# Kernel optimization log

Measured on AMD Instinct MI355X. Metric: run time of the kernel, lower is better.

Reference implementation:

```python
import jax, jax.numpy as jnp
import numpy as np

H = 1024      # hidden_size
NH = 16       # num_heads
HD = H // NH  # head_dim
MLP_DIM = 4096
EPS = 1e-6


def setup_inputs() -> dict:
    key = jax.random.key(0)
    ks = jax.random.split(key, 16)
    B, S = 8, 1024
    s_in = 1.0 / np.sqrt(H)
    s_mlp = 1.0 / np.sqrt(MLP_DIM)
    return {
        "x": jax.random.normal(ks[0], (B, S, H), jnp.float32),
        "ln1_g": jnp.ones((H,), jnp.float32),
        "ln1_b": jnp.zeros((H,), jnp.float32),
        "Wq": jax.random.normal(ks[1], (H, H), jnp.float32) * s_in,
        "bq": jnp.zeros((H,), jnp.float32),
        "Wk": jax.random.normal(ks[2], (H, H), jnp.float32) * s_in,
        "bk": jnp.zeros((H,), jnp.float32),
        "Wv": jax.random.normal(ks[3], (H, H), jnp.float32) * s_in,
        "bv": jnp.zeros((H,), jnp.float32),
        "Wo": jax.random.normal(ks[4], (H, H), jnp.float32) * s_in,
        "bo": jnp.zeros((H,), jnp.float32),
        "ln2_g": jnp.ones((H,), jnp.float32),
        "ln2_b": jnp.zeros((H,), jnp.float32),
        "W1": jax.random.normal(ks[5], (H, MLP_DIM), jnp.float32) * s_in,
        "b1": jnp.zeros((MLP_DIM,), jnp.float32),
        "W2": jax.random.normal(ks[6], (MLP_DIM, H), jnp.float32) * s_mlp,
        "b2": jnp.zeros((H,), jnp.float32),
    }


def _layernorm(x, g, b):
    mu = jnp.mean(x, axis=-1, keepdims=True)
    var = jnp.mean(jnp.square(x - mu), axis=-1, keepdims=True)
    return (x - mu) * jax.lax.rsqrt(var + EPS) * g + b


def reference(x, ln1_g, ln1_b, Wq, bq, Wk, bk, Wv, bv, Wo, bo,
              ln2_g, ln2_b, W1, b1, W2, b2):
    B, S, _ = x.shape
    # pre-LN attention
    h = _layernorm(x, ln1_g, ln1_b)
    q = (h @ Wq + bq).reshape(B, S, NH, HD).transpose(0, 2, 1, 3)  # bhsd
    k = (h @ Wk + bk).reshape(B, S, NH, HD).transpose(0, 2, 1, 3)
    v = (h @ Wv + bv).reshape(B, S, NH, HD).transpose(0, 2, 1, 3)
    scale = HD ** -0.5
    scores = jnp.einsum('bhqd,bhkd->bhqk', q, k) * scale
    weights = jax.nn.softmax(scores, axis=-1)
    attended = jnp.einsum('bhqk,bhkd->bhqd', weights, v)
    attended = attended.transpose(0, 2, 1, 3).reshape(B, S, H)
    x = x + attended @ Wo + bo
    # pre-LN MLP
    h = _layernorm(x, ln2_g, ln2_b)
    h = jax.nn.gelu(h @ W1 + b1, approximate=False)
    x = x + h @ W2 + b2
    return x
```

## Files before the change

### kernel.cpp

```cpp
#include <hip/hip_runtime.h>

#define H_DIM 1024
#define NHEADS 16
#define HD 64
#define SEQ 1024
#define BATCH 8
#define ROWS (BATCH*SEQ)
#define MLPD 4096

typedef __bf16 bf16x8 __attribute__((ext_vector_type(8)));
typedef float f32x4 __attribute__((ext_vector_type(4)));

__device__ __forceinline__ unsigned short f2bf(float f) {
    unsigned u = __float_as_uint(f);
    unsigned r = u + 0x7FFFu + ((u >> 16) & 1u);
    return (unsigned short)(r >> 16);
}

__global__ void transpose_all(const float* __restrict__ Wq, const float* __restrict__ Wk,
                              const float* __restrict__ Wv, const float* __restrict__ Wo,
                              const float* __restrict__ W1, const float* __restrict__ W2,
                              unsigned short* __restrict__ WqT, unsigned short* __restrict__ WkT,
                              unsigned short* __restrict__ WvT, unsigned short* __restrict__ WoT,
                              unsigned short* __restrict__ W1T, unsigned short* __restrict__ W2T)
{
    __shared__ float tile[32][33];
    const int id = blockIdx.x;
    const float* in; unsigned short* outp; int K, N, t;
    if (id < 4096) {
        const int wsel = id >> 10; t = id & 1023;
        in   = (wsel == 0) ? Wq  : (wsel == 1) ? Wk  : (wsel == 2) ? Wv  : Wo;
        outp = (wsel == 0) ? WqT : (wsel == 1) ? WkT : (wsel == 2) ? WvT : WoT;
        K = 1024; N = 1024;
    } else if (id < 8192) {
        t = id - 4096; in = W1; outp = W1T; K = 1024; N = 4096;
    } else {
        t = id - 8192; in = W2; outp = W2T; K = 4096; N = 1024;
    }
    const int ntx = N >> 5;
    const int n0 = (t % ntx) * 32, k0 = (t / ntx) * 32;
    const int tx = threadIdx.x, ty = threadIdx.y;
    #pragma unroll
    for (int i = ty; i < 32; i += 8)
        tile[i][tx] = in[(size_t)(k0 + i) * N + n0 + tx];
    __syncthreads();
    #pragma unroll
    for (int i = ty; i < 32; i += 8)
        outp[(size_t)(n0 + i) * K + k0 + tx] = f2bf(tile[tx][i]);
}

__global__ void transpose_v(const unsigned short* __restrict__ in,
                            unsigned short* __restrict__ out)
{
    __shared__ unsigned short tile[32][33];
    const size_t base = (size_t)blockIdx.z * (SEQ * HD);
    const int d0 = blockIdx.x * 32, s0 = blockIdx.y * 32;
    const int tx = threadIdx.x, ty = threadIdx.y;
    #pragma unroll
    for (int i = ty; i < 32; i += 8)
        tile[i][tx] = in[base + (size_t)(s0 + i) * HD + d0 + tx];
    __syncthreads();
    const int fx = ((tx & 12) << 1) | ((tx & 16) >> 2) | (tx & 3);
    #pragma unroll
    for (int i = ty; i < 32; i += 8)
        out[base + (size_t)(d0 + i) * SEQ + s0 + fx] = tile[tx][i];
}

__global__ __launch_bounds__(256) void ln_kernel(const float* __restrict__ x,
    const float* __restrict__ g, const float* __restrict__ b,
    unsigned short* __restrict__ out)
{
    __shared__ float red[4];
    const int row = blockIdx.x;
    const int tid = threadIdx.x;
    const float4 v = *(const float4*)(x + (size_t)row * H_DIM + tid * 4);
    float s = v.x + v.y + v.z + v.w;
    #pragma unroll
    for (int off = 32; off >= 1; off >>= 1) s += __shfl_xor(s, off);
    if ((tid & 63) == 0) red[tid >> 6] = s;
    __syncthreads();
    const float mu = (red[0] + red[1] + red[2] + red[3]) * (1.0f / H_DIM);
    __syncthreads();
    const float dx = v.x - mu, dy = v.y - mu, dz = v.z - mu, dw = v.w - mu;
    float q = dx * dx + dy * dy + dz * dz + dw * dw;
    #pragma unroll
    for (int off = 32; off >= 1; off >>= 1) q += __shfl_xor(q, off);
    if ((tid & 63) == 0) red[tid >> 6] = q;
    __syncthreads();
    const float var = (red[0] + red[1] + red[2] + red[3]) * (1.0f / H_DIM);
    const float rstd = rsqrtf(var + 1e-6f);
    const float4 gv = *(const float4*)(g + tid * 4);
    const float4 bv = *(const float4*)(b + tid * 4);
    ushort4 o;
    o.x = f2bf(dx * rstd * gv.x + bv.x);
    o.y = f2bf(dy * rstd * gv.y + bv.y);
    o.z = f2bf(dz * rstd * gv.z + bv.z);
    o.w = f2bf(dw * rstd * gv.w + bv.w);
    *(ushort4*)(out + (size_t)row * H_DIM + tid * 4) = o;
}

template<int MODE>
__global__ __launch_bounds__(256) void gemm_dp(
    const unsigned short* __restrict__ A, const unsigned short* __restrict__ Bt,
    const float* __restrict__ bias0, const float* __restrict__ bias1,
    const float* __restrict__ bias2, const float* resid,
    float* outF, unsigned short* __restrict__ outH,
    int N, int K, int gn)
{
    __shared__ __align__(16) unsigned short As[128 * 128];
    __shared__ __align__(16) unsigned short Bs[128 * 128];

    const int tid = threadIdx.x, lane = tid & 63;
    const int w = tid >> 6;
    const int wm = w >> 1, wn = w & 1;

    const int nwg = gridDim.x;
    const int swzb = (blockIdx.x & 7) * (nwg >> 3) + (blockIdx.x >> 3);
    const int bm = swzb / gn, bn = swzb % gn;

    const int srow = tid >> 4;
    const int sc = (tid & 15) ^ (srow & 7);
    const unsigned short* Abase = A  + (size_t)(bm * 128) * K;
    const unsigned short* Bbase = Bt + (size_t)(bn * 128) * K;

    auto stage = [&](int kt) {
        const size_t kofs = (size_t)kt * 128 + sc * 8;
        #pragma unroll
        for (int q = 0; q < 8; ++q)
            __builtin_amdgcn_global_load_lds(
                (__attribute__((address_space(1))) void*)(Abase + (size_t)(q * 16 + srow) * K + kofs),
                (__attribute__((address_space(3))) void*)(&As[q * 2048 + tid * 8]), 16, 0, 0);
        #pragma unroll
        for (int q = 0; q < 8; ++q)
            __builtin_amdgcn_global_load_lds(
                (__attribute__((address_space(1))) void*)(Bbase + (size_t)(q * 16 + srow) * K + kofs),
                (__attribute__((address_space(3))) void*)(&Bs[q * 2048 + tid * 8]), 16, 0, 0);
    };

    const int lr = lane & 15, hk = lane >> 4, sx = lr & 7;
    const int arow = (wm * 64 + lr) * 128;
    const int brow = (wn * 64 + lr) * 128;

    f32x4 acc[4][4] = {};
    const int nkt = K >> 7;

    for (int t = 0; t < nkt; ++t) {
        stage(t);
        __syncthreads();

        const unsigned short* Ab = &As[arow];
        const unsigned short* Bb = &Bs[brow];

        #pragma unroll
        for (int ks = 0; ks < 4; ++ks) {
            const int px = ((ks * 4 + hk) ^ sx) * 8;
            bf16x8 a[4], b[4];
            #pragma unroll
            for (int i = 0; i < 4; ++i) { b[i] = *(const bf16x8*)(Bb + i * 2048 + px);
                                          a[i] = *(const bf16x8*)(Ab + i * 2048 + px); }
            __builtin_amdgcn_s_setprio(1);
            #pragma unroll
            for (int mi = 0; mi < 4; ++mi)
                #pragma unroll
                for (int ni = 0; ni < 4; ++ni)
                    acc[mi][ni] = __builtin_amdgcn_mfma_f32_16x16x32_bf16(a[mi], b[ni], acc[mi][ni], 0, 0, 0);
            __builtin_amdgcn_s_setprio(0);
        }
        __syncthreads();
    }

    #pragma unroll
    for (int mi = 0; mi < 4; ++mi) {
        #pragma unroll
        for (int ni = 0; ni < 4; ++ni) {
            const int gcol = bn * 128 + wn * 64 + ni * 16 + lr;
            #pragma unroll
            for (int r = 0; r < 4; ++r) {
                const int grow = bm * 128 + wm * 64 + mi * 16 + hk * 4 + r;
                if (MODE == 0) {
                    const int which = gcol >> 10;
                    const int col = gcol & 1023;
                    const float* bp = (which == 0) ? bias0 : (which == 1) ? bias1 : bias2;
                    const float v = acc[mi][ni][r] + bp[col];
                    const int b_ = grow >> 10, s_ = grow & 1023, h_ = col >> 6, d_ = col & 63;
                    outH[(size_t)which * (ROWS * 1024) +
                         (size_t)(b_ * NHEADS + h_) * 65536 + s_ * 64 + d_] = f2bf(v);
                } else if (MODE == 2) {
                    const float v = acc[mi][ni][r] + bias0[gcol];
                    const size_t idx = (size_t)grow * N + gcol;
                    outF[idx] = resid[idx] + v;
                }
            }
        }
    }
}

template<int MODE, int BN>
__global__ __launch_bounds__(512) void gemm_kp(
    const unsigned short* __restrict__ A, const unsigned short* __restrict__ Bt,
    const float* __restrict__ bias0, const float* __restrict__ bias1,
    const float* __restrict__ bias2, const float* resid,
    float* outF, unsigned short* __restrict__ outH,
    int N, int K, int gn)
{
    constexpr int WN = (BN == 256) ? 4 : 2;
    constexpr int WM = 8 / WN;
    constexpr int RM = 256 / WM;
    constexpr int RN = BN / WN;
    constexpr int MR = RM / 16;
    constexpr int NR = RN / 16;
    constexpr int BJ = BN / 128;

    __shared__ __align__(16) unsigned short As[2][2][8192];
    __shared__ __align__(16) unsigned short Bs[2][2][BN * 32];

    const int tid = threadIdx.x, lane = tid & 63;
    const int w = tid >> 6;
    const int wm = w / WN, wn = w % WN;

    const int nwg = gridDim.x;
    const int swzb = (blockIdx.x & 7) * (nwg >> 3) + (blockIdx.x >> 3);
    const int bm = swzb / gn, bn = swzb % gn;

    const unsigned short* Abase = A  + (size_t)(bm * 256) * K;
    const unsigned short* Bbase = Bt + (size_t)(bn * BN) * K;

    int asrow[2], asoff[2];
    #pragma unroll
    for (int j = 0; j < 2; ++j) {
        const int slot = j * 512 + tid;
        asrow[j] = slot >> 2;
        asoff[j] = ((slot & 3) ^ ((asrow[j] >> 1) & 3)) * 8;
    }
    int bsrow[BJ], bsoff[BJ];
    #pragma unroll
    for (int j = 0; j < BJ; ++j) {
        const int slot = j * 512 + tid;
        bsrow[j] = slot >> 2;
        bsoff[j] = ((slot & 3) ^ ((bsrow[j] >> 1) & 3)) * 8;
    }

    auto stageKH = [&](int buf, int kt, int s) {
        #pragma unroll
        for (int j = 0; j < 2; ++j)
            __builtin_amdgcn_global_load_lds(
                (__attribute__((address_space(1))) void*)(Abase + (size_t)asrow[j] * K + (size_t)kt * 64 + s * 32 + asoff[j]),
                (__attribute__((address_space(3))) void*)(&As[buf][s][(j * 512 + tid) * 8]), 16, 0, 0);
        #pragma unroll
        for (int j = 0; j < BJ; ++j)
            __builtin_amdgcn_global_load_lds(
                (__attribute__((address_space(1))) void*)(Bbase + (size_t)bsrow[j] * K + (size_t)kt * 64 + s * 32 + bsoff[j]),
                (__attribute__((address_space(3))) void*)(&Bs[buf][s][(j * 512 + tid) * 8]), 16, 0, 0);
    };

    const int lr = lane & 15, hk = lane >> 4;
    int aoff[MR], boff[NR];
    #pragma unroll
    for (int mf = 0; mf < MR; ++mf) {
        const int R = wm * RM + mf * 16 + lr;
        aoff[mf] = R * 32 + ((hk ^ ((R >> 1) & 3)) * 8);
    }
    #pragma unroll
    for (int nf = 0; nf < NR; ++nf) {
        const int R = wn * RN + nf * 16 + lr;
        boff[nf] = R * 32 + ((hk ^ ((R >> 1) & 3)) * 8);
    }

    f32x4 acc[MR][NR] = {};
    const int nkt = K >> 6;

    stageKH(0, 0, 0);
    stageKH(0, 0, 1);
    if constexpr (BJ == 2) asm volatile("s_waitcnt vmcnt(4)" ::: "memory");
    else                   asm volatile("s_waitcnt vmcnt(3)" ::: "memory");
    __builtin_amdgcn_s_barrier();
    asm volatile("" ::: "memory");

    for (int t = 0; t < nkt; ++t) {
        const int buf = t & 1;
        #pragma unroll
        for (int s = 0; s < 2; ++s) {
            const unsigned short* Ar = &As[buf][s][0];
            const unsigned short* Br = &Bs[buf][s][0];
            bf16x8 af[MR], bf[NR];
            #pragma unroll
            for (int nf = 0; nf < NR; ++nf) bf[nf] = *(const bf16x8*)(Br + boff[nf]);
            #pragma unroll
            for (int mf = 0; mf < MR; ++mf) af[mf] = *(const bf16x8*)(Ar + aoff[mf]);

            if (t + 1 < nkt) {
                stageKH(buf ^ 1, t + 1, s);
                if constexpr (BJ == 2) asm volatile("s_waitcnt vmcnt(4)" ::: "memory");
                else                   asm volatile("s_waitcnt vmcnt(3)" ::: "memory");
            } else {
                asm volatile("s_waitcnt vmcnt(0)" ::: "memory");
            }
            __builtin_amdgcn_s_barrier();
            asm volatile("" ::: "memory");

            __builtin_amdgcn_s_setprio(1);
            #pragma unroll
            for (int mf = 0; mf < MR; ++mf)
                #pragma unroll
                for (int nf = 0; nf < NR; ++nf)
                    acc[mf][nf] = __builtin_amdgcn_mfma_f32_16x16x32_bf16(af[mf], bf[nf], acc[mf][nf], 0, 0, 0);
            __builtin_amdgcn_s_setprio(0);
        }
    }

    #pragma unroll
    for (int mf = 0; mf < MR; ++mf) {
        #pragma unroll
        for (int nf = 0; nf < NR; ++nf) {
            const int gcol = bn * BN + wn * RN + nf * 16 + lr;
            #pragma unroll
            for (int r = 0; r < 4; ++r) {
                const int grow = bm * 256 + wm * RM + mf * 16 + hk * 4 + r;
                if (MODE == 0) {
                    const int which = gcol >> 10;
                    const int col = gcol & 1023;
                    const float* bp = (which == 0) ? bias0 : (which == 1) ? bias1 : bias2;
                    const float v = acc[mf][nf][r] + bp[col];
                    const int b_ = grow >> 10, s_ = grow & 1023, h_ = col >> 6, d_ = col & 63;
                    outH[(size_t)which * (ROWS * 1024) +
                         (size_t)(b_ * NHEADS + h_) * 65536 + s_ * 64 + d_] = f2bf(v);
                } else if (MODE == 2) {
                    const float v = acc[mf][nf][r] + bias0[gcol];
                    const size_t idx = (size_t)grow * N + gcol;
                    outF[idx] = resid[idx] + v;
                } else {
                    const float v = acc[mf][nf][r] + bias0[gcol];
                    const float t3 = fmaf(0.044715f * v * v, v, v);
                    const float e  = __builtin_amdgcn_exp2f(-2.3022086f * t3);
                    const float ge = v * __builtin_amdgcn_rcpf(1.0f + e);
                    outH[(size_t)grow * N + gcol] = f2bf(ge);
                }
            }
        }
    }
}

__global__ __launch_bounds__(256) void attn_kernel(const unsigned short* __restrict__ q,
    const unsigned short* __restrict__ k, const unsigned short* __restrict__ vT,
    unsigned short* __restrict__ out)
{
    __shared__ __align__(16) unsigned short Ks[2][4096];
    __shared__ __align__(16) unsigned short Vs[2][4096];
    const int tid = threadIdx.x, lane = tid & 63, w = tid >> 6;
    const int bh = blockIdx.y;
    const int q0 = blockIdx.x * 256;
    const size_t headBase = (size_t)bh * (SEQ * HD);

    const int qr = lane & 15;
    bf16x8 qf[4][2];
    #pragma unroll
    for (int g = 0; g < 4; ++g) {
        const unsigned short* qp = q + headBase
            + (size_t)(q0 + w * 64 + g * 16 + qr) * HD + (lane >> 4) * 8;
        qf[g][0] = *(const bf16x8*)(qp);
        qf[g][1] = *(const bf16x8*)(qp + 32);
    }

    float lacc[4] = {0.f, 0.f, 0.f, 0.f};
    f32x4 oacc[4][4] = {};

    const int srow = tid >> 3;
    const int swz  = ((tid & 7) ^ (srow & 7)) * 8;
    const int pc   = (lane >> 4) ^ (lane & 7);

    auto stage = [&](int buf, int kt) {
        #pragma unroll
        for (int s = 0; s < 2; ++s) {
            const unsigned short* gk = k  + headBase + (size_t)(kt + s * 32 + srow) * HD + swz;
            const unsigned short* gv = vT + headBase + (size_t)(s * 32 + srow) * SEQ + kt + swz;
            __builtin_amdgcn_global_load_lds((__attribute__((address_space(1))) void*)gk,
                (__attribute__((address_space(3))) void*)(&Ks[buf][s * 2048 + w * 512]), 16, 0, 0);
            __builtin_amdgcn_global_load_lds((__attribute__((address_space(1))) void*)gv,
                (__attribute__((address_space(3))) void*)(&Vs[buf][s * 2048 + w * 512]), 16, 0, 0);
        }
    };

    stage(0, 0);
    __syncthreads();

    const float C1 = 0.125f * 1.44269504f;
    const float C2 = -4.0f * 1.44269504f;

    for (int t = 0; t < 16; ++t) {
        const int cur = t & 1;
        if (t < 15) stage(cur ^ 1, (t + 1) * 64);

        const unsigned short* KB = &Ks[cur][0];
        const unsigned short* VB = &Vs[cur][0];

        #pragma unroll
        for (int g = 0; g < 4; ++g) {
            f32x4 s4[4] = {};
            __builtin_amdgcn_s_setprio(1);
            #pragma unroll
            for (int ni = 0; ni < 4; ++ni) {
                const unsigned short* pk = KB + (ni * 16 + qr) * 64;
                s4[ni] = __builtin_amdgcn_mfma_f32_16x16x32_bf16(*(const bf16x8*)(pk + pc * 8),       qf[g][0], s4[ni], 0, 0, 0);
                s4[ni] = __builtin_amdgcn_mfma_f32_16x16x32_bf16(*(const bf16x8*)(pk + (pc ^ 4) * 8), qf[g][1], s4[ni], 0, 0, 0);
            }
            __builtin_amdgcn_s_setprio(0);

            unsigned U[4][2];
            float ls = 0.f;
            #pragma unroll
            for (int ni = 0; ni < 4; ++ni) {
                const float p0 = __builtin_amdgcn_exp2f(fmaf(s4[ni][0], C1, C2));
                const float p1 = __builtin_amdgcn_exp2f(fmaf(s4[ni][1], C1, C2));
                const float p2 = __builtin_amdgcn_exp2f(fmaf(s4[ni][2], C1, C2));
                const float p3 = __builtin_amdgcn_exp2f(fmaf(s4[ni][3], C1, C2));
                ls += (p0 + p1) + (p2 + p3);
                asm("v_cvt_pk_bf16_f32 %0, %1, %2" : "=v"(U[ni][0]) : "v"(p0), "v"(p1));
                asm("v_cvt_pk_bf16_f32 %0, %1, %2" : "=v"(U[ni][1]) : "v"(p2), "v"(p3));
            }
            lacc[g] += ls;

            union { unsigned u[4]; bf16x8 v; } W0, W1;
            W0.u[0] = U[0][0]; W0.u[1] = U[0][1]; W0.u[2] = U[1][0]; W0.u[3] = U[1][1];
            W1.u[0] = U[2][0]; W1.u[1] = U[2][1]; W1.u[2] = U[3][0]; W1.u[3] = U[3][1];

            __builtin_amdgcn_s_setprio(1);
            #pragma unroll
            for (int nd = 0; nd < 4; ++nd) {
                const unsigned short* pv = VB + (nd * 16 + qr) * 64;
                oacc[g][nd] = __builtin_amdgcn_mfma_f32_16x16x32_bf16(*(const bf16x8*)(pv + pc * 8),       W0.v, oacc[g][nd], 0, 0, 0);
                oacc[g][nd] = __builtin_amdgcn_mfma_f32_16x16x32_bf16(*(const bf16x8*)(pv + (pc ^ 4) * 8), W1.v, oacc[g][nd], 0, 0, 0);
            }
            __builtin_amdgcn_s_setprio(0);
        }

        __syncthreads();
    }

    const int b_ = bh >> 4, h_ = bh & 15;
    const int hh = (lane >> 4) * 4;
    #pragma unroll
    for (int g = 0; g < 4; ++g) {
        float l = lacc[g];
        l += __shfl_xor(l, 16);
        l += __shfl_xor(l, 32);
        const float inv = 1.0f / l;
        const int s_ = q0 + w * 64 + g * 16 + qr;
        #pragma unroll
        for (int nd = 0; nd < 4; ++nd) {
            ushort4 o;
            o.x = f2bf(oacc[g][nd][0] * inv);
            o.y = f2bf(oacc[g][nd][1] * inv);
            o.z = f2bf(oacc[g][nd][2] * inv);
            o.w = f2bf(oacc[g][nd][3] * inv);
            *(ushort4*)(out + (size_t)(b_ * SEQ + s_) * H_DIM + h_ * 64 + nd * 16 + hh) = o;
        }
    }
}

extern "C" void kernel_launch(void* const* d_in, const int* in_sizes, int n_in,
                              void* d_out, int out_size, void* d_ws, size_t ws_size,
                              hipStream_t stream)
{
    const float* x    = (const float*)d_in[0];
    const float* ln1g = (const float*)d_in[1];
    const float* ln1b = (const float*)d_in[2];
    const float* Wq   = (const float*)d_in[3];
    const float* bq   = (const float*)d_in[4];
    const float* Wk   = (const float*)d_in[5];
    const float* bk   = (const float*)d_in[6];
    const float* Wv   = (const float*)d_in[7];
    const float* bv   = (const float*)d_in[8];
    const float* Wo   = (const float*)d_in[9];
    const float* bo   = (const float*)d_in[10];
    const float* ln2g = (const float*)d_in[11];
    const float* ln2b = (const float*)d_in[12];
    const float* W1   = (const float*)d_in[13];
    const float* b1   = (const float*)d_in[14];
    const float* W2   = (const float*)d_in[15];
    const float* b2   = (const float*)d_in[16];
    float* out = (float*)d_out;

    char* ws = (char*)d_ws;
    const size_t MB = 1024 * 1024;
    unsigned short* h1  = (unsigned short*)(ws);
    unsigned short* qb  = (unsigned short*)(ws + 16 * MB);
    unsigned short* kb  = (unsigned short*)(ws + 32 * MB);
    unsigned short* vb  = (unsigned short*)(ws + 48 * MB);
    unsigned short* vTb = (unsigned short*)(ws + 64 * MB);
    unsigned short* mlp = (unsigned short*)(ws + 16 * MB);
    unsigned short* ao  = h1;
    unsigned short* WqT = (unsigned short*)(ws + 80 * MB);
    unsigned short* WkT = (unsigned short*)(ws + 82 * MB);
    unsigned short* WvT = (unsigned short*)(ws + 84 * MB);
    unsigned short* WoT = (unsigned short*)(ws + 86 * MB);
    unsigned short* W1T = (unsigned short*)(ws + 88 * MB);
    unsigned short* W2T = (unsigned short*)(ws + 96 * MB);

    transpose_all<<<12288, dim3(32, 8), 0, stream>>>(Wq, Wk, Wv, Wo, W1, W2,
                                                     WqT, WkT, WvT, WoT, W1T, W2T);

    ln_kernel<<<ROWS, 256, 0, stream>>>(x, ln1g, ln1b, h1);

    gemm_kp<0, 256><<<384, 512, 0, stream>>>(h1, WqT, bq, bk, bv, nullptr, nullptr, qb, 3072, 1024, 12);

    transpose_v<<<dim3(2, 32, 128), dim3(32, 8), 0, stream>>>(vb, vTb);

    attn_kernel<<<dim3(4, 128), 256, 0, stream>>>(qb, kb, vTb, ao);

    gemm_dp<2><<<512, 256, 0, stream>>>(ao, WoT, bo, bo, bo, x, out, nullptr, 1024, 1024, 8);

    ln_kernel<<<ROWS, 256, 0, stream>>>(out, ln2g, ln2b, h1);

    gemm_kp<3, 256><<<512, 512, 0, stream>>>(h1, W1T, b1, b1, b1, nullptr, nullptr, mlp, 4096, 1024, 16);
    gemm_dp<2><<<512, 256, 0, stream>>>(mlp, W2T, b2, b2, b2, out, out, nullptr, 1024, 4096, 8);
}
```

Before: 345.6 us.

## Replace double-buffered GEMM with four-slot K=32 pipeline for QKV and MLP-up

```diff
diff --git a/kernel.cpp b/kernel.cpp
--- a/kernel.cpp
+++ b/kernel.cpp
@@ -177,15 +177,7 @@
             #pragma unroll
             for (int r = 0; r < 4; ++r) {
                 const int grow = bm * 128 + wm * 64 + mi * 16 + hk * 4 + r;
-                if (MODE == 0) {
-                    const int which = gcol >> 10;
-                    const int col = gcol & 1023;
-                    const float* bp = (which == 0) ? bias0 : (which == 1) ? bias1 : bias2;
-                    const float v = acc[mi][ni][r] + bp[col];
-                    const int b_ = grow >> 10, s_ = grow & 1023, h_ = col >> 6, d_ = col & 63;
-                    outH[(size_t)which * (ROWS * 1024) +
-                         (size_t)(b_ * NHEADS + h_) * 65536 + s_ * 64 + d_] = f2bf(v);
-                } else if (MODE == 2) {
+                if (MODE == 2) {
                     const float v = acc[mi][ni][r] + bias0[gcol];
                     const size_t idx = (size_t)grow * N + gcol;
                     outF[idx] = resid[idx] + v;
@@ -195,127 +187,107 @@
     }
 }
 
-template<int MODE, int BN>
-__global__ __launch_bounds__(512) void gemm_kp(
+template<int MODE>
+__global__ __launch_bounds__(512) void gemm_kp4(
     const unsigned short* __restrict__ A, const unsigned short* __restrict__ Bt,
     const float* __restrict__ bias0, const float* __restrict__ bias1,
-    const float* __restrict__ bias2, const float* resid,
-    float* outF, unsigned short* __restrict__ outH,
-    int N, int K, int gn)
-{
-    constexpr int WN = (BN == 256) ? 4 : 2;
-    constexpr int WM = 8 / WN;
-    constexpr int RM = 256 / WM;
-    constexpr int RN = BN / WN;
-    constexpr int MR = RM / 16;
-    constexpr int NR = RN / 16;
-    constexpr int BJ = BN / 128;
-
-    __shared__ __align__(16) unsigned short As[2][2][8192];
-    __shared__ __align__(16) unsigned short Bs[2][2][BN * 32];
+    const float* __restrict__ bias2,
+    unsigned short* __restrict__ outH, int N, int K, int gn)
+{
+    __shared__ __align__(16) unsigned short As[4][8192];
+    __shared__ __align__(16) unsigned short Bs[4][8192];
 
     const int tid = threadIdx.x, lane = tid & 63;
     const int w = tid >> 6;
-    const int wm = w / WN, wn = w % WN;
+    const int wm = w >> 2, wn = w & 3;
 
     const int nwg = gridDim.x;
     const int swzb = (blockIdx.x & 7) * (nwg >> 3) + (blockIdx.x >> 3);
     const int bm = swzb / gn, bn = swzb % gn;
 
     const unsigned short* Abase = A  + (size_t)(bm * 256) * K;
-    const unsigned short* Bbase = Bt + (size_t)(bn * BN) * K;
-
-    int asrow[2], asoff[2];
+    const unsigned short* Bbase = Bt + (size_t)(bn * 256) * K;
+
+    int srow[2], soff[2];
     #pragma unroll
     for (int j = 0; j < 2; ++j) {
         const int slot = j * 512 + tid;
-        asrow[j] = slot >> 2;
-        asoff[j] = ((slot & 3) ^ ((asrow[j] >> 1) & 3)) * 8;
-    }
-    int bsrow[BJ], bsoff[BJ];
-    #pragma unroll
-    for (int j = 0; j < BJ; ++j) {
-        const int slot = j * 512 + tid;
-        bsrow[j] = slot >> 2;
-        bsoff[j] = ((slot & 3) ^ ((bsrow[j] >> 1) & 3)) * 8;
-    }
-
-    auto stageKH = [&](int buf, int kt, int s) {
-        #pragma unroll
-        for (int j = 0; j < 2; ++j)
+        srow[j] = slot >> 2;
+        soff[j] = ((slot & 3) ^ ((srow[j] >> 1) & 3)) * 8;
+    }
+
+    auto stage = [&](int sl, int kt) {
+        #pragma unroll
+        for (int j = 0; j < 2; ++j) {
+            const size_t off = (size_t)srow[j] * K + (size_t)kt * 32 + soff[j];
             __builtin_amdgcn_global_load_lds(
-                (__attribute__((address_space(1))) void*)(Abase + (size_t)asrow[j] * K + (size_t)kt * 64 + s * 32 + asoff[j]),
-                (__attribute__((address_space(3))) void*)(&As[buf][s][(j * 512 + tid) * 8]), 16, 0, 0);
-        #pragma unroll
-        for (int j = 0; j < BJ; ++j)
+                (__attribute__((address_space(1))) void*)(Abase + off),
+                (__attribute__((address_space(3))) void*)(&As[sl][(j * 512 + tid) * 8]), 16, 0, 0);
             __builtin_amdgcn_global_load_lds(
-                (__attribute__((address_space(1))) void*)(Bbase + (size_t)bsrow[j] * K + (size_t)kt * 64 + s * 32 + bsoff[j]),
-                (__attribute__((address_space(3))) void*)(&Bs[buf][s][(j * 512 + tid) * 8]), 16, 0, 0);
+                (__attribute__((address_space(1))) void*)(Bbase + off),
+                (__attribute__((address_space(3))) void*)(&Bs[sl][(j * 512 + tid) * 8]), 16, 0, 0);
+        }
     };
 
     const int lr = lane & 15, hk = lane >> 4;
-    int aoff[MR], boff[NR];
-    #pragma unroll
-    for (int mf = 0; mf < MR; ++mf) {
-        const int R = wm * RM + mf * 16 + lr;
+    int aoff[8], boff[4];
+    #pragma unroll
+    for (int mf = 0; mf < 8; ++mf) {
+        const int R = wm * 128 + mf * 16 + lr;
         aoff[mf] = R * 32 + ((hk ^ ((R >> 1) & 3)) * 8);
     }
     #pragma unroll
-    for (int nf = 0; nf < NR; ++nf) {
-        const int R = wn * RN + nf * 16 + lr;
+    for (int nf = 0; nf < 4; ++nf) {
+        const int R = wn * 64 + nf * 16 + lr;
         boff[nf] = R * 32 + ((hk ^ ((R >> 1) & 3)) * 8);
     }
 
-    f32x4 acc[MR][NR] = {};
-    const int nkt = K >> 6;
-
-    stageKH(0, 0, 0);
-    stageKH(0, 0, 1);
-    if constexpr (BJ == 2) asm volatile("s_waitcnt vmcnt(4)" ::: "memory");
-    else                   asm volatile("s_waitcnt vmcnt(3)" ::: "memory");
+    f32x4 acc[8][4] = {};
+    const int nkt = K >> 5;
+
+    stage(0, 0); stage(1, 1); stage(2, 2);
+    asm volatile("s_waitcnt vmcnt(8)" ::: "memory");
     __builtin_amdgcn_s_barrier();
     asm volatile("" ::: "memory");
 
     for (int t = 0; t < nkt; ++t) {
-        const int buf = t & 1;
-        #pragma unroll
-        for (int s = 0; s < 2; ++s) {
-            const unsigned short* Ar = &As[buf][s][0];
-            const unsigned short* Br = &Bs[buf][s][0];
-            bf16x8 af[MR], bf[NR];
-            #pragma unroll
-            for (int nf = 0; nf < NR; ++nf) bf[nf] = *(const bf16x8*)(Br + boff[nf]);
-            #pragma unroll
-            for (int mf = 0; mf < MR; ++mf) af[mf] = *(const bf16x8*)(Ar + aoff[mf]);
-
-            if (t + 1 < nkt) {
-                stageKH(buf ^ 1, t + 1, s);
-                if constexpr (BJ == 2) asm volatile("s_waitcnt vmcnt(4)" ::: "memory");
-                else                   asm volatile("s_waitcnt vmcnt(3)" ::: "memory");
-            } else {
-                asm volatile("s_waitcnt vmcnt(0)" ::: "memory");
-            }
-            __builtin_amdgcn_s_barrier();
-            asm volatile("" ::: "memory");
-
-            __builtin_amdgcn_s_setprio(1);
-            #pragma unroll
-            for (int mf = 0; mf < MR; ++mf)
-                #pragma unroll
-                for (int nf = 0; nf < NR; ++nf)
-                    acc[mf][nf] = __builtin_amdgcn_mfma_f32_16x16x32_bf16(af[mf], bf[nf], acc[mf][nf], 0, 0, 0);
-            __builtin_amdgcn_s_setprio(0);
-        }
-    }
-
-    #pragma unroll
-    for (int mf = 0; mf < MR; ++mf) {
-        #pragma unroll
-        for (int nf = 0; nf < NR; ++nf) {
-            const int gcol = bn * BN + wn * RN + nf * 16 + lr;
+        const int sl = t & 3;
+        const unsigned short* Ar = &As[sl][0];
+        const unsigned short* Br = &Bs[sl][0];
+        bf16x8 af[8], bf[4];
+        #pragma unroll
+        for (int nf = 0; nf < 4; ++nf) bf[nf] = *(const bf16x8*)(Br + boff[nf]);
+        #pragma unroll
+        for (int mf = 0; mf < 8; ++mf) af[mf] = *(const bf16x8*)(Ar + aoff[mf]);
+
+        if (t + 3 < nkt) {
+            stage((t + 3) & 3, t + 3);
+            asm volatile("s_waitcnt vmcnt(8)" ::: "memory");
+        } else if (t + 3 == nkt) {
+            asm volatile("s_waitcnt vmcnt(4)" ::: "memory");
+        } else {
+            asm volatile("s_waitcnt vmcnt(0)" ::: "memory");
+        }
+        __builtin_amdgcn_s_barrier();
+        asm volatile("" ::: "memory");
+
+        __builtin_amdgcn_s_setprio(1);
+        #pragma unroll
+        for (int mf = 0; mf < 8; ++mf)
+            #pragma unroll
+            for (int nf = 0; nf < 4; ++nf)
+                acc[mf][nf] = __builtin_amdgcn_mfma_f32_16x16x32_bf16(af[mf], bf[nf], acc[mf][nf], 0, 0, 0);
+        __builtin_amdgcn_s_setprio(0);
+    }
+
+    #pragma unroll
+    for (int mf = 0; mf < 8; ++mf) {
+        #pragma unroll
+        for (int nf = 0; nf < 4; ++nf) {
+            const int gcol = bn * 256 + wn * 64 + nf * 16 + lr;
             #pragma unroll
             for (int r = 0; r < 4; ++r) {
-                const int grow = bm * 256 + wm * RM + mf * 16 + hk * 4 + r;
+                const int grow = bm * 256 + wm * 128 + mf * 16 + hk * 4 + r;
                 if (MODE == 0) {
                     const int which = gcol >> 10;
                     const int col = gcol & 1023;
@@ -324,10 +296,6 @@
                     const int b_ = grow >> 10, s_ = grow & 1023, h_ = col >> 6, d_ = col & 63;
                     outH[(size_t)which * (ROWS * 1024) +
                          (size_t)(b_ * NHEADS + h_) * 65536 + s_ * 64 + d_] = f2bf(v);
-                } else if (MODE == 2) {
-                    const float v = acc[mf][nf][r] + bias0[gcol];
-                    const size_t idx = (size_t)grow * N + gcol;
-                    outF[idx] = resid[idx] + v;
                 } else {
                     const float v = acc[mf][nf][r] + bias0[gcol];
                     const float t3 = fmaf(0.044715f * v * v, v, v);
@@ -501,7 +469,7 @@
 
     ln_kernel<<<ROWS, 256, 0, stream>>>(x, ln1g, ln1b, h1);
 
-    gemm_kp<0, 256><<<384, 512, 0, stream>>>(h1, WqT, bq, bk, bv, nullptr, nullptr, qb, 3072, 1024, 12);
+    gemm_kp4<0><<<384, 512, 0, stream>>>(h1, WqT, bq, bk, bv, qb, 3072, 1024, 12);
 
     transpose_v<<<dim3(2, 32, 128), dim3(32, 8), 0, stream>>>(vb, vTb);
 
@@ -511,6 +479,6 @@
 
     ln_kernel<<<ROWS, 256, 0, stream>>>(out, ln2g, ln2b, h1);
 
-    gemm_kp<3, 256><<<512, 512, 0, stream>>>(h1, W1T, b1, b1, b1, nullptr, nullptr, mlp, 4096, 1024, 16);
+    gemm_kp4<3><<<512, 512, 0, stream>>>(h1, W1T, b1, b1, b1, mlp, 4096, 1024, 16);
     gemm_dp<2><<<512, 256, 0, stream>>>(mlp, W2T, b2, b2, b2, out, out, nullptr, 1024, 4096, 8);
 }
```

After: 346.9 us. Within noise of the previous version (+0.4%).
